# Performance work log

Hardware: AMD Instinct MI355X
Metric: run time of the kernel (lower is better)

Reference implementation:

```python
import jax, jax.numpy as jnp
import numpy as np

N = 512
E = N * N
H = 64          # hidden_dim
ED = 6          # edge_dim
L = 4           # n_layers
EPS = 1e-5


def _lin(key, fan_in, fan_out):
    k1, k2 = jax.random.split(key)
    w = jax.random.normal(k1, (fan_in, fan_out), jnp.float32) / np.sqrt(fan_in)
    b = jax.random.normal(k2, (fan_out,), jnp.float32) * 0.01
    return w, b


def _lin_stack(key, fan_in, fan_out, n):
    ws, bs = zip(*[_lin(jax.random.fold_in(key, i), fan_in, fan_out) for i in range(n)])
    return jnp.stack(ws), jnp.stack(bs)


def setup_inputs() -> dict:
    key = jax.random.key(0)
    ks = jax.random.split(key, 16)
    idx = jnp.arange(N, dtype=jnp.int32)
    src = jnp.repeat(idx, N)          # x_j source nodes
    dst = jnp.tile(idx, N)            # x_i target nodes (aggregation index)
    edge_index = jnp.stack([src, dst])  # [2, E]
    x = jax.random.normal(ks[0], (N, 6), jnp.float32)
    edge_attr = jax.random.normal(ks[1], (E, ED), jnp.float32)
    enc_w1, enc_b1 = _lin(ks[2], 6, H)
    enc_w2, enc_b2 = _lin(ks[3], H, H)
    att_w1, att_b1 = _lin_stack(ks[4], 2 * H + ED, H, L)   # [L,134,64]
    att_w2, att_b2 = _lin_stack(ks[5], H, 1, L)
    val_w1, val_b1 = _lin_stack(ks[6], H + ED, H, L)       # [L,70,64]
    val_w2, val_b2 = _lin_stack(ks[7], H, H, L)
    upd_w1, upd_b1 = _lin_stack(ks[8], 2 * H, H, L)        # [L,128,64]
    upd_w2, upd_b2 = _lin_stack(ks[9], H, H, L)
    ln_g = jnp.ones((L, H), jnp.float32)
    ln_b = jnp.zeros((L, H), jnp.float32)
    dec_w1, dec_b1 = _lin(ks[10], H, H)
    dec_w2, dec_b2 = _lin(ks[11], H, 1)
    return dict(x=x, edge_attr=edge_attr,
                enc_w1=enc_w1, enc_b1=enc_b1, enc_w2=enc_w2, enc_b2=enc_b2,
                att_w1=att_w1, att_b1=att_b1, att_w2=att_w2, att_b2=att_b2,
                val_w1=val_w1, val_b1=val_b1, val_w2=val_w2, val_b2=val_b2,
                upd_w1=upd_w1, upd_b1=upd_b1, upd_w2=upd_w2, upd_b2=upd_b2,
                ln_g=ln_g, ln_b=ln_b,
                dec_w1=dec_w1, dec_b1=dec_b1, dec_w2=dec_w2, dec_b2=dec_b2,
                edge_index=edge_index)


def reference(x, edge_attr, enc_w1, enc_b1, enc_w2, enc_b2,
              att_w1, att_b1, att_w2, att_b2,
              val_w1, val_b1, val_w2, val_b2,
              upd_w1, upd_b1, upd_w2, upd_b2,
              ln_g, ln_b, dec_w1, dec_b1, dec_w2, dec_b2, edge_index):
    src, dst = edge_index[0], edge_index[1]
    h = jax.nn.relu(x @ enc_w1 + enc_b1) @ enc_w2 + enc_b2  # [N,H]
    for l in range(L):
        hi = h[dst]                           # x_i  [E,H]
        hj = h[src]                           # x_j  [E,H]
        # attention logits: MLP([x_i || x_j || e])
        a_in = jnp.concatenate([hi, hj, edge_attr], axis=-1)   # [E,2H+ED]
        a = jax.nn.leaky_relu(a_in @ att_w1[l] + att_b1[l], 0.2) @ att_w2[l] + att_b2[l]
        a = a[:, 0]                                            # [E]
        # segment softmax over destination index (numerically stable)
        m = jax.ops.segment_max(a, dst, num_segments=N)
        e = jnp.exp(a - m[dst])
        s = jax.ops.segment_sum(e, dst, num_segments=N)
        alpha = e / s[dst]                                     # [E]
        # values: MLP([x_j || e])
        v_in = jnp.concatenate([hj, edge_attr], axis=-1)       # [E,H+ED]
        v = jax.nn.relu(v_in @ val_w1[l] + val_b1[l]) @ val_w2[l] + val_b2[l]
        agg = jax.ops.segment_sum(v * alpha[:, None], dst, num_segments=N)  # [N,H]
        # update + residual + LayerNorm
        u_in = jnp.concatenate([h, agg], axis=-1)              # [N,2H]
        u = jax.nn.relu(u_in @ upd_w1[l] + upd_b1[l]) @ upd_w2[l] + upd_b2[l]
        r = u + h
        mu = jnp.mean(r, axis=-1, keepdims=True)
        var = jnp.mean((r - mu) ** 2, axis=-1, keepdims=True)
        h = ln_g[l] * (r - mu) / jnp.sqrt(var + EPS) + ln_b[l]
    return jax.nn.relu(h @ dec_w1 + dec_b1) @ dec_w2 + dec_b2  # [N,1]
```

## Files before the change

### kernel.cpp

```cpp
#include <hip/hip_runtime.h>
#include <math.h>

#define NN 512
#define HH 64
#define NLAYERS 4
#define LN_EPS 1e-5f


__launch_bounds__(256)
__global__ void k_pre(const float* __restrict__ ea, const float* __restrict__ x,
                      const float* __restrict__ ew1, const float* __restrict__ eb1,
                      const float* __restrict__ ew2, const float* __restrict__ eb2,
                      const float* __restrict__ aw1, const float* __restrict__ ab1,
                      const float* __restrict__ wa2, const float* __restrict__ vw1,
                      const float* __restrict__ vb1,
                      float* __restrict__ EAT, float* __restrict__ h,
                      float* __restrict__ Pd, float* __restrict__ Qs,
                      float* __restrict__ Rv, float* __restrict__ Sq) {
    __shared__ float r1[HH], hs[HH];
    __shared__ float part[4][HH], partQ[4][HH], partR[4][HH];

    if (blockIdx.x < 1024) {
        int t = blockIdx.x * 256 + threadIdx.x;
        int i = t & (NN - 1);
        int j = t >> 9;
        const float2* s2 = (const float2*)(ea + ((size_t)i * NN + j) * 6);
        float2 e0 = s2[0], e1 = s2[1], e2 = s2[2];
        float4 a, b;
        a.x = e0.x; a.y = e0.y; a.z = e1.x; a.w = e1.y;
        b.x = e2.x; b.y = e2.y; b.z = 0.f; b.w = 0.f;
        float4* dst = (float4*)(EAT + (size_t)t * 8);
        dst[0] = a;
        dst[1] = b;
        return;
    }

    const int j = blockIdx.x - 1024;
    const int tid = threadIdx.x;
    const int d = tid & 63;
    const int w = tid >> 6;

    if (w == 0) {
        float z = eb1[d];
#pragma unroll
        for (int k = 0; k < 6; ++k) z += x[j * 6 + k] * ew1[k * HH + d];
        r1[d] = fmaxf(z, 0.f);
    }
    __syncthreads();
    {
        float z2 = (w == 0) ? eb2[d] : 0.f;
        for (int k = w * 16; k < w * 16 + 16; ++k) z2 += r1[k] * ew2[k * HH + d];
        part[w][d] = z2;
    }
    __syncthreads();
    if (w == 0) {
        float hv = part[0][d] + part[1][d] + part[2][d] + part[3][d];
        h[(size_t)j * HH + d] = hv;
        hs[d] = hv;
    }
    __syncthreads();
    {
        float pp = (w == 0) ? ab1[d] : 0.f;
        float qq = 0.f;
        float rr = (w == 0) ? vb1[d] : 0.f;
        for (int k = w * 16; k < w * 16 + 16; ++k) {
            float hk = hs[k];
            pp += hk * aw1[k * HH + d];
            qq += hk * aw1[(HH + k) * HH + d];
            rr += hk * vw1[k * HH + d];
        }
        part[w][d] = pp; partQ[w][d] = qq; partR[w][d] = rr;
    }
    __syncthreads();
    if (w == 0) {
        float qf = partQ[0][d] + partQ[1][d] + partQ[2][d] + partQ[3][d];
        Pd[(size_t)j * HH + d] = part[0][d] + part[1][d] + part[2][d] + part[3][d];
        Qs[(size_t)j * HH + d] = qf;
        Rv[(size_t)j * HH + d] = partR[0][d] + partR[1][d] + partR[2][d] + partR[3][d];
        float sq = qf * wa2[d];
#pragma unroll
        for (int o = 32; o; o >>= 1) sq += __shfl_xor(sq, o);
        if (d == 0) Sq[j] = sq;
    }
}

__launch_bounds__(512, 4)
__global__ void k_layer(const float* __restrict__ eat, const float* __restrict__ h_in,
                        const float* __restrict__ Pd, const float* __restrict__ Qs,
                        const float* __restrict__ Rv, const float* __restrict__ Sq,
                        const float* __restrict__ waE,
                        const float* __restrict__ wa2v,
                        const float* __restrict__ wvE,
                        const float* __restrict__ wv2, const float* __restrict__ vb2,
                        const float* __restrict__ uw1, const float* __restrict__ ub1,
                        const float* __restrict__ uw2, const float* __restrict__ ub2,
                        const float* __restrict__ lng, const float* __restrict__ lnb,
                        float* __restrict__ h_out,
                        const float* __restrict__ aw1n, const float* __restrict__ ab1n,
                        const float* __restrict__ wa2n, const float* __restrict__ vw1n,
                        const float* __restrict__ vb1n,
                        float* __restrict__ Pdn, float* __restrict__ Qsn,
                        float* __restrict__ Rvn, float* __restrict__ Sqn,
                        const float* __restrict__ dw1, const float* __restrict__ db1,
                        const float* __restrict__ dw2, const float* __restrict__ db2,
                        float* __restrict__ out,
                        int do_prep) {
    const int j = blockIdx.x;
    const int tid = threadIdx.x;
    const int lane = tid & 63;
    const int w = tid >> 6;
    const int slot = lane >> 3;
    const int dp = lane & 7;
    const int d0 = dp * 8;
    const int d = lane;

    __shared__ __align__(16) float ea_s[NN * 8];
    __shared__ __align__(16) float Sq_s[NN];
    __shared__ float a_s[NN];
    __shared__ float red_m[8], red_s[8];
    __shared__ float accs[8][HH];
    __shared__ float av[HH], uin[2 * HH], r1[HH], hs[HH];
    __shared__ float part[8][HH], partQ[8][HH], partR[8][HH];

    {
        const float4* s4 = (const float4*)(eat + (size_t)j * (NN * 8));
        float4* d4 = (float4*)ea_s;
        d4[tid] = s4[tid];
        d4[tid + 512] = s4[tid + 512];
    }
    if (tid < 128) ((float4*)Sq_s)[tid] = ((const float4*)Sq)[tid];

    float WA[6][8], wa2raw[8], wa2r[8], pdr[8], w6s[6];
#pragma unroll
    for (int k = 0; k < 6; ++k)
#pragma unroll
        for (int u = 0; u < 8; ++u) WA[k][u] = waE[k * HH + d0 + u];
#pragma unroll
    for (int u = 0; u < 8; ++u) {
        wa2raw[u] = wa2v[d0 + u];
        pdr[u] = Pd[(size_t)j * HH + d0 + u];
    }
#pragma unroll
    for (int k = 0; k < 6; ++k) {
        float t = 0.f;
#pragma unroll
        for (int u = 0; u < 8; ++u) t += WA[k][u] * wa2raw[u];
        t += __shfl_xor(t, 1);
        t += __shfl_xor(t, 2);
        t += __shfl_xor(t, 4);
        w6s[k] = 0.6f * t;
    }
#pragma unroll
    for (int u = 0; u < 8; ++u) wa2r[u] = 0.4f * wa2raw[u];
    __syncthreads();

    {
        float alin = 0.6f * Sq_s[tid];
#pragma unroll
        for (int k = 0; k < 6; ++k) alin += ea_s[tid * 8 + k] * w6s[k];
        __syncthreads();
        Sq_s[tid] = alin;
    }
    __syncthreads();

    const int ibw = w * 64;
    float lmax = -1e30f;
#pragma unroll
    for (int it = 0; it < 8; ++it) {
        const int i = ibw + it * 8 + slot;
        const float4* q4 = (const float4*)(Qs + (size_t)i * HH + d0);
        float4 qa = q4[0], qb = q4[1];
        float qv[8] = {qa.x, qa.y, qa.z, qa.w, qb.x, qb.y, qb.z, qb.w};
        const float4* e4 = (const float4*)(ea_s + i * 8);
        float4 ea0 = e4[0], ea1 = e4[1];
        float eav[6] = {ea0.x, ea0.y, ea0.z, ea0.w, ea1.x, ea1.y};
        float p1 = 0.f;
#pragma unroll
        for (int u = 0; u < 8; ++u) {
            float z = pdr[u] + qv[u];
#pragma unroll
            for (int k = 0; k < 6; ++k) z += eav[k] * WA[k][u];
            p1 += fabsf(z) * wa2r[u];
        }
        p1 += __shfl_xor(p1, 1);
        p1 += __shfl_xor(p1, 2);
        p1 += __shfl_xor(p1, 4);
        float a = Sq_s[i] + p1;
        if (dp == 0) a_s[i] = a;
        lmax = fmaxf(lmax, a);
    }
#pragma unroll
    for (int o = 32; o; o >>= 1) lmax = fmaxf(lmax, __shfl_xor(lmax, o));
    if (lane == 0) red_m[w] = lmax;
    __syncthreads();
    float m = red_m[0];
#pragma unroll
    for (int q = 1; q < 8; ++q) m = fmaxf(m, red_m[q]);

    float e = expf(a_s[tid] - m);
    a_s[tid] = e;
    float lsum = e;
#pragma unroll
    for (int o = 32; o; o >>= 1) lsum += __shfl_xor(lsum, o);
    if (lane == 0) red_s[w] = lsum;
    __syncthreads();
    float s = red_s[0];
#pragma unroll
    for (int q = 1; q < 8; ++q) s += red_s[q];

    float WV[6][8];
#pragma unroll
    for (int k = 0; k < 6; ++k)
#pragma unroll
        for (int u = 0; u < 8; ++u) WV[k][u] = wvE[k * HH + d0 + u];
    float acc[8] = {0.f, 0.f, 0.f, 0.f, 0.f, 0.f, 0.f, 0.f};
#pragma unroll
    for (int it = 0; it < 8; ++it) {
        const int i = ibw + it * 8 + slot;
        const float4* r4 = (const float4*)(Rv + (size_t)i * HH + d0);
        float4 ra = r4[0], rb = r4[1];
        float rv[8] = {ra.x, ra.y, ra.z, ra.w, rb.x, rb.y, rb.z, rb.w};
        const float4* e4 = (const float4*)(ea_s + i * 8);
        float4 ea0 = e4[0], ea1 = e4[1];
        float eav[6] = {ea0.x, ea0.y, ea0.z, ea0.w, ea1.x, ea1.y};
        const float wi = a_s[i];
#pragma unroll
        for (int u = 0; u < 8; ++u) {
            float z = rv[u];
#pragma unroll
            for (int k = 0; k < 6; ++k) z += eav[k] * WV[k][u];
            acc[u] += wi * fmaxf(z, 0.f);
        }
    }
#pragma unroll
    for (int u = 0; u < 8; ++u) {
        acc[u] += __shfl_xor(acc[u], 8);
        acc[u] += __shfl_xor(acc[u], 16);
        acc[u] += __shfl_xor(acc[u], 32);
    }
    if (slot == 0) {
#pragma unroll
        for (int u = 0; u < 8; ++u) accs[w][d0 + u] = acc[u];
    }
    __syncthreads();
    if (tid < HH) {
        float tot = accs[0][tid];
#pragma unroll
        for (int q = 1; q < 8; ++q) tot += accs[q][tid];
        av[tid] = tot / s;
    }
    __syncthreads();

    const float hv = h_in[(size_t)j * HH + d];
    {
        float p = (w == 0) ? vb2[d] : 0.f;
        for (int k = w * 8; k < w * 8 + 8; ++k) p += av[k] * wv2[k * HH + d];
        part[w][d] = p;
        if (w == 0) uin[d] = hv;
    }
    __syncthreads();
    if (w == 0) {
        float agg = part[0][d];
#pragma unroll
        for (int q = 1; q < 8; ++q) agg += part[q][d];
        uin[HH + d] = agg;
    }
    __syncthreads();
    {
        float t = (w == 0) ? ub1[d] : 0.f;
        for (int c = w * 16; c < w * 16 + 16; ++c) t += uin[c] * uw1[c * HH + d];
        part[w][d] = t;
    }
    __syncthreads();
    if (w == 0) {
        float t = part[0][d];
#pragma unroll
        for (int q = 1; q < 8; ++q) t += part[q][d];
        r1[d] = fmaxf(t, 0.f);
    }
    __syncthreads();
    {
        float u = (w == 0) ? ub2[d] : 0.f;
        for (int k = w * 8; k < w * 8 + 8; ++k) u += r1[k] * uw2[k * HH + d];
        part[w][d] = u;
    }
    __syncthreads();
    if (w == 0) {
        float r = hv + part[0][d];
#pragma unroll
        for (int q = 1; q < 8; ++q) r += part[q][d];
        float sum = r;
#pragma unroll
        for (int o = 32; o; o >>= 1) sum += __shfl_xor(sum, o);
        float mu = sum * (1.f / HH);
        float dr = r - mu;
        float v2 = dr * dr;
#pragma unroll
        for (int o = 32; o; o >>= 1) v2 += __shfl_xor(v2, o);
        float var = v2 * (1.f / HH);
        float hn = lng[d] * dr * (1.f / sqrtf(var + LN_EPS)) + lnb[d];
        h_out[(size_t)j * HH + d] = hn;
        hs[d] = hn;
    }
    __syncthreads();

    if (do_prep) {
        float pp = (w == 0) ? ab1n[d] : 0.f;
        float qq = 0.f;
        float rr = (w == 0) ? vb1n[d] : 0.f;
        for (int k = w * 8; k < w * 8 + 8; ++k) {
            float hk = hs[k];
            pp += hk * aw1n[k * HH + d];
            qq += hk * aw1n[(HH + k) * HH + d];
            rr += hk * vw1n[k * HH + d];
        }
        part[w][d] = pp; partQ[w][d] = qq; partR[w][d] = rr;
        __syncthreads();
        if (w == 0) {
            float pf = part[0][d], qf = partQ[0][d], rf = partR[0][d];
#pragma unroll
            for (int q = 1; q < 8; ++q) {
                pf += part[q][d]; qf += partQ[q][d]; rf += partR[q][d];
            }
            Pdn[(size_t)j * HH + d] = pf;
            Qsn[(size_t)j * HH + d] = qf;
            Rvn[(size_t)j * HH + d] = rf;
            float sq = qf * wa2n[d];
#pragma unroll
            for (int o = 32; o; o >>= 1) sq += __shfl_xor(sq, o);
            if (d == 0) Sqn[j] = sq;
        }
    } else {
        float t = (w == 0) ? db1[d] : 0.f;
        for (int k = w * 8; k < w * 8 + 8; ++k) t += hs[k] * dw1[k * HH + d];
        part[w][d] = t;
        __syncthreads();
        if (w == 0) {
            float tt = part[0][d];
#pragma unroll
            for (int q = 1; q < 8; ++q) tt += part[q][d];
            tt = fmaxf(tt, 0.f);
            float sum = tt * dw2[d];
#pragma unroll
            for (int o = 32; o; o >>= 1) sum += __shfl_xor(sum, o);
            if (d == 0) out[j] = sum + db2[0];
        }
    }
}

extern "C" void kernel_launch(void* const* d_in, const int* in_sizes, int n_in,
                              void* d_out, int out_size, void* d_ws, size_t ws_size,
                              hipStream_t stream) {
    const float* x      = (const float*)d_in[0];
    const float* ea     = (const float*)d_in[1];
    const float* enc_w1 = (const float*)d_in[2];
    const float* enc_b1 = (const float*)d_in[3];
    const float* enc_w2 = (const float*)d_in[4];
    const float* enc_b2 = (const float*)d_in[5];
    const float* att_w1 = (const float*)d_in[6];
    const float* att_b1 = (const float*)d_in[7];
    const float* att_w2 = (const float*)d_in[8];
    const float* val_w1 = (const float*)d_in[10];
    const float* val_b1 = (const float*)d_in[11];
    const float* val_w2 = (const float*)d_in[12];
    const float* val_b2 = (const float*)d_in[13];
    const float* upd_w1 = (const float*)d_in[14];
    const float* upd_b1 = (const float*)d_in[15];
    const float* upd_w2 = (const float*)d_in[16];
    const float* upd_b2 = (const float*)d_in[17];
    const float* ln_g   = (const float*)d_in[18];
    const float* ln_b   = (const float*)d_in[19];
    const float* dec_w1 = (const float*)d_in[20];
    const float* dec_b1 = (const float*)d_in[21];
    const float* dec_w2 = (const float*)d_in[22];
    const float* dec_b2 = (const float*)d_in[23];

    const size_t NH = (size_t)NN * HH;
    float* ws   = (float*)d_ws;
    float* EAT  = ws;
    float* h0   = EAT + (size_t)NN * NN * 8;
    float* h1   = h0 + NH;
    float* Pd0  = h1 + NH;
    float* Pd1  = Pd0 + NH;
    float* Qs0  = Pd1 + NH;
    float* Qs1  = Qs0 + NH;
    float* Rv0  = Qs1 + NH;
    float* Rv1  = Rv0 + NH;
    float* Sq0  = Rv1 + NH;
    float* Sq1  = Sq0 + NN;

    float* Pdb[2] = {Pd0, Pd1};
    float* Qsb[2] = {Qs0, Qs1};
    float* Rvb[2] = {Rv0, Rv1};
    float* Sqb[2] = {Sq0, Sq1};
    float* hb[2]  = {h0, h1};

    k_pre<<<1536, 256, 0, stream>>>(ea, x, enc_w1, enc_b1, enc_w2, enc_b2,
                                    att_w1, att_b1, att_w2, val_w1, val_b1,
                                    EAT, h0, Pd0, Qs0, Rv0, Sq0);

    for (int l = 0; l < NLAYERS; ++l) {
        const int cur = l & 1, nxt = (l + 1) & 1;
        const int np = (l + 1 < NLAYERS) ? (l + 1) : l;
        const float* aw1 = att_w1 + (size_t)l * 134 * HH;
        const float* vw1 = val_w1 + (size_t)l * 70 * HH;
        k_layer<<<NN, 512, 0, stream>>>(
            EAT, hb[cur],
            Pdb[cur], Qsb[cur], Rvb[cur], Sqb[cur],
            aw1 + 128 * HH, att_w2 + l * HH, vw1 + 64 * HH,
            val_w2 + (size_t)l * HH * HH, val_b2 + l * HH,
            upd_w1 + (size_t)l * 2 * HH * HH, upd_b1 + l * HH,
            upd_w2 + (size_t)l * HH * HH, upd_b2 + l * HH,
            ln_g + l * HH, ln_b + l * HH,
            hb[nxt],
            att_w1 + (size_t)np * 134 * HH, att_b1 + np * HH, att_w2 + np * HH,
            val_w1 + (size_t)np * 70 * HH, val_b1 + np * HH,
            Pdb[nxt], Qsb[nxt], Rvb[nxt], Sqb[nxt],
            dec_w1, dec_b1, dec_w2, dec_b2, (float*)d_out,
            (l + 1 < NLAYERS) ? 1 : 0);
    }
}
```

Measured before the change: 209.4 us.

## Fuse all layers into one persistent cooperative kernel with grid sync

```diff
diff --git a/kernel.cpp b/kernel.cpp
--- a/kernel.cpp
+++ b/kernel.cpp
@@ -1,5 +1,8 @@
 #include <hip/hip_runtime.h>
+#include <hip/hip_cooperative_groups.h>
 #include <math.h>
+
+namespace cg = cooperative_groups;
 
 #define NN 512
 #define HH 64
@@ -84,12 +87,289 @@
     }
 }
 
+struct NetP {
+    const float *EAT, *h0, *Pd0;
+    const float *aw1, *ab1, *aw2, *vw1, *vb1, *vw2, *vb2;
+    const float *uw1, *ub1, *uw2, *ub2, *lng, *lnb;
+    const float *dw1, *db1, *dw2, *db2;
+    float *Qs0, *Qs1, *Rv0, *Rv1, *Sq0, *Sq1;
+    float *out;
+};
+
+__launch_bounds__(512, 4)
+__global__ void k_net(NetP P) {
+    cg::grid_group grid = cg::this_grid();
+    const int j = blockIdx.x;
+    const int tid = threadIdx.x;
+    const int lane = tid & 63;
+    const int w = tid >> 6;
+    const int slot = lane >> 3;
+    const int dp = lane & 7;
+    const int d0 = dp * 8;
+    const int d = lane;
+
+    __shared__ __align__(16) float ea_s[NN * 8];
+    __shared__ __align__(16) float Sq_s[NN];
+    __shared__ float a_s[NN];
+    __shared__ float red_m[8], red_s[8];
+    __shared__ float accs[8][HH];
+    __shared__ float av[HH], uin[2 * HH], r1[HH], hs[HH], pd_s[HH];
+    __shared__ float part[8][HH], partQ[8][HH], partR[8][HH];
+
+    {
+        const float4* s4 = (const float4*)(P.EAT + (size_t)j * (NN * 8));
+        float4* d4 = (float4*)ea_s;
+        d4[tid] = s4[tid];
+        d4[tid + 512] = s4[tid + 512];
+    }
+    if (w == 0) {
+        hs[d] = P.h0[(size_t)j * HH + d];
+        pd_s[d] = P.Pd0[(size_t)j * HH + d];
+    }
+    __syncthreads();
+
+    for (int l = 0; l < NLAYERS; ++l) {
+        const float* aw1l = P.aw1 + (size_t)l * 134 * HH;
+        const float* waE  = aw1l + 128 * HH;
+        const float* wa2v = P.aw2 + l * HH;
+        const float* wvE  = P.vw1 + (size_t)l * 70 * HH + 64 * HH;
+        const float* Qs_c = (l & 1) ? P.Qs1 : P.Qs0;
+        const float* Rv_c = (l & 1) ? P.Rv1 : P.Rv0;
+        const float* Sq_c = (l & 1) ? P.Sq1 : P.Sq0;
+
+        if (tid < 128) ((float4*)Sq_s)[tid] = ((const float4*)Sq_c)[tid];
+
+        float WA[6][8], wa2raw[8], wa2r[8], pdr[8], w6s[6];
+#pragma unroll
+        for (int k = 0; k < 6; ++k)
+#pragma unroll
+            for (int u = 0; u < 8; ++u) WA[k][u] = waE[k * HH + d0 + u];
+#pragma unroll
+        for (int u = 0; u < 8; ++u) {
+            wa2raw[u] = wa2v[d0 + u];
+            pdr[u] = pd_s[d0 + u];
+        }
+#pragma unroll
+        for (int k = 0; k < 6; ++k) {
+            float t = 0.f;
+#pragma unroll
+            for (int u = 0; u < 8; ++u) t += WA[k][u] * wa2raw[u];
+            t += __shfl_xor(t, 1);
+            t += __shfl_xor(t, 2);
+            t += __shfl_xor(t, 4);
+            w6s[k] = 0.6f * t;
+        }
+#pragma unroll
+        for (int u = 0; u < 8; ++u) wa2r[u] = 0.4f * wa2raw[u];
+        __syncthreads();
+
+        {
+            float alin = 0.6f * Sq_s[tid];
+#pragma unroll
+            for (int k = 0; k < 6; ++k) alin += ea_s[tid * 8 + k] * w6s[k];
+            a_s[tid] = alin;
+        }
+        __syncthreads();
+
+        const int ibw = w * 64;
+        float lmax = -1e30f;
+#pragma unroll
+        for (int it = 0; it < 8; ++it) {
+            const int i = ibw + it * 8 + slot;
+            const float4* q4 = (const float4*)(Qs_c + (size_t)i * HH + d0);
+            float4 qa = q4[0], qb = q4[1];
+            float qv[8] = {qa.x, qa.y, qa.z, qa.w, qb.x, qb.y, qb.z, qb.w};
+            const float4* e4 = (const float4*)(ea_s + i * 8);
+            float4 ea0 = e4[0], ea1 = e4[1];
+            float eav[6] = {ea0.x, ea0.y, ea0.z, ea0.w, ea1.x, ea1.y};
+            float p1 = 0.f;
+#pragma unroll
+            for (int u = 0; u < 8; ++u) {
+                float z = pdr[u] + qv[u];
+#pragma unroll
+                for (int k = 0; k < 6; ++k) z += eav[k] * WA[k][u];
+                p1 += fabsf(z) * wa2r[u];
+            }
+            p1 += __shfl_xor(p1, 1);
+            p1 += __shfl_xor(p1, 2);
+            p1 += __shfl_xor(p1, 4);
+            float a = a_s[i] + p1;
+            if (dp == 0) a_s[i] = a;
+            lmax = fmaxf(lmax, a);
+        }
+#pragma unroll
+        for (int o = 32; o; o >>= 1) lmax = fmaxf(lmax, __shfl_xor(lmax, o));
+        if (lane == 0) red_m[w] = lmax;
+        __syncthreads();
+        float m = red_m[0];
+#pragma unroll
+        for (int q = 1; q < 8; ++q) m = fmaxf(m, red_m[q]);
+
+        float e = expf(a_s[tid] - m);
+        a_s[tid] = e;
+        float lsum = e;
+#pragma unroll
+        for (int o = 32; o; o >>= 1) lsum += __shfl_xor(lsum, o);
+        if (lane == 0) red_s[w] = lsum;
+        __syncthreads();
+        float s = red_s[0];
+#pragma unroll
+        for (int q = 1; q < 8; ++q) s += red_s[q];
+
+        float WV[6][8];
+#pragma unroll
+        for (int k = 0; k < 6; ++k)
+#pragma unroll
+            for (int u = 0; u < 8; ++u) WV[k][u] = wvE[k * HH + d0 + u];
+        float acc[8] = {0.f, 0.f, 0.f, 0.f, 0.f, 0.f, 0.f, 0.f};
+#pragma unroll
+        for (int it = 0; it < 8; ++it) {
+            const int i = ibw + it * 8 + slot;
+            const float4* r4 = (const float4*)(Rv_c + (size_t)i * HH + d0);
+            float4 ra = r4[0], rb = r4[1];
+            float rv[8] = {ra.x, ra.y, ra.z, ra.w, rb.x, rb.y, rb.z, rb.w};
+            const float4* e4 = (const float4*)(ea_s + i * 8);
+            float4 ea0 = e4[0], ea1 = e4[1];
+            float eav[6] = {ea0.x, ea0.y, ea0.z, ea0.w, ea1.x, ea1.y};
+            const float wi = a_s[i];
+#pragma unroll
+            for (int u = 0; u < 8; ++u) {
+                float z = rv[u];
+#pragma unroll
+                for (int k = 0; k < 6; ++k) z += eav[k] * WV[k][u];
+                acc[u] += wi * fmaxf(z, 0.f);
+            }
+        }
+#pragma unroll
+        for (int u = 0; u < 8; ++u) {
+            acc[u] += __shfl_xor(acc[u], 8);
+            acc[u] += __shfl_xor(acc[u], 16);
+            acc[u] += __shfl_xor(acc[u], 32);
+        }
+        if (slot == 0) {
+#pragma unroll
+            for (int u = 0; u < 8; ++u) accs[w][d0 + u] = acc[u];
+        }
+        __syncthreads();
+        if (tid < HH) {
+            float tot = accs[0][tid];
+#pragma unroll
+            for (int q = 1; q < 8; ++q) tot += accs[q][tid];
+            av[tid] = tot / s;
+        }
+        __syncthreads();
+
+        const float* wv2 = P.vw2 + (size_t)l * HH * HH;
+        const float* uw1 = P.uw1 + (size_t)l * 2 * HH * HH;
+        const float* uw2 = P.uw2 + (size_t)l * HH * HH;
+        const float hv = hs[d];
+        {
+            float p = (w == 0) ? P.vb2[l * HH + d] : 0.f;
+            for (int k = w * 8; k < w * 8 + 8; ++k) p += av[k] * wv2[k * HH + d];
+            part[w][d] = p;
+            if (w == 0) uin[d] = hv;
+        }
+        __syncthreads();
+        if (w == 0) {
+            float agg = part[0][d];
+#pragma unroll
+            for (int q = 1; q < 8; ++q) agg += part[q][d];
+            uin[HH + d] = agg;
+        }
+        __syncthreads();
+        {
+            float t = (w == 0) ? P.ub1[l * HH + d] : 0.f;
+            for (int c = w * 16; c < w * 16 + 16; ++c) t += uin[c] * uw1[c * HH + d];
+            part[w][d] = t;
+        }
+        __syncthreads();
+        if (w == 0) {
+            float t = part[0][d];
+#pragma unroll
+            for (int q = 1; q < 8; ++q) t += part[q][d];
+            r1[d] = fmaxf(t, 0.f);
+        }
+        __syncthreads();
+        {
+            float u = (w == 0) ? P.ub2[l * HH + d] : 0.f;
+            for (int k = w * 8; k < w * 8 + 8; ++k) u += r1[k] * uw2[k * HH + d];
+            part[w][d] = u;
+        }
+        __syncthreads();
+        if (w == 0) {
+            float r = hv + part[0][d];
+#pragma unroll
+            for (int q = 1; q < 8; ++q) r += part[q][d];
+            float sum = r;
+#pragma unroll
+            for (int o = 32; o; o >>= 1) sum += __shfl_xor(sum, o);
+            float mu = sum * (1.f / HH);
+            float dr = r - mu;
+            float v2 = dr * dr;
+#pragma unroll
+            for (int o = 32; o; o >>= 1) v2 += __shfl_xor(v2, o);
+            float var = v2 * (1.f / HH);
+            hs[d] = P.lng[l * HH + d] * dr * (1.f / sqrtf(var + LN_EPS)) + P.lnb[l * HH + d];
+        }
+        __syncthreads();
+
+        if (l + 1 < NLAYERS) {
+            const int np = l + 1;
+            const float* aw1n = P.aw1 + (size_t)np * 134 * HH;
+            const float* vw1n = P.vw1 + (size_t)np * 70 * HH;
+            float* Qsn = (np & 1) ? P.Qs1 : P.Qs0;
+            float* Rvn = (np & 1) ? P.Rv1 : P.Rv0;
+            float* Sqn = (np & 1) ? P.Sq1 : P.Sq0;
+            float pp = (w == 0) ? P.ab1[np * HH + d] : 0.f;
+            float qq = 0.f;
+            float rr = (w == 0) ? P.vb1[np * HH + d] : 0.f;
+            for (int k = w * 8; k < w * 8 + 8; ++k) {
+                float hk = hs[k];
+                pp += hk * aw1n[k * HH + d];
+                qq += hk * aw1n[(HH + k) * HH + d];
+                rr += hk * vw1n[k * HH + d];
+            }
+            part[w][d] = pp; partQ[w][d] = qq; partR[w][d] = rr;
+            __syncthreads();
+            if (w == 0) {
+                float pf = part[0][d], qf = partQ[0][d], rf = partR[0][d];
+#pragma unroll
+                for (int q = 1; q < 8; ++q) {
+                    pf += part[q][d]; qf += partQ[q][d]; rf += partR[q][d];
+                }
+                pd_s[d] = pf;
+                Qsn[(size_t)j * HH + d] = qf;
+                Rvn[(size_t)j * HH + d] = rf;
+                float sq = qf * P.aw2[np * HH + d];
+#pragma unroll
+                for (int o = 32; o; o >>= 1) sq += __shfl_xor(sq, o);
+                if (d == 0) Sqn[j] = sq;
+            }
+            grid.sync();
+        } else {
+            float t = (w == 0) ? P.db1[d] : 0.f;
+            for (int k = w * 8; k < w * 8 + 8; ++k) t += hs[k] * P.dw1[k * HH + d];
+            part[w][d] = t;
+            __syncthreads();
+            if (w == 0) {
+                float tt = part[0][d];
+#pragma unroll
+                for (int q = 1; q < 8; ++q) tt += part[q][d];
+                tt = fmaxf(tt, 0.f);
+                float sum = tt * P.dw2[d];
+#pragma unroll
+                for (int o = 32; o; o >>= 1) sum += __shfl_xor(sum, o);
+                if (d == 0) P.out[j] = sum + P.db2[0];
+            }
+        }
+    }
+}
+
 __launch_bounds__(512, 4)
 __global__ void k_layer(const float* __restrict__ eat, const float* __restrict__ h_in,
                         const float* __restrict__ Pd, const float* __restrict__ Qs,
                         const float* __restrict__ Rv, const float* __restrict__ Sq,
-                        const float* __restrict__ waE,
-                        const float* __restrict__ wa2v,
+                        const float* __restrict__ waE, const float* __restrict__ wa2v,
                         const float* __restrict__ wvE,
                         const float* __restrict__ wv2, const float* __restrict__ vb2,
                         const float* __restrict__ uw1, const float* __restrict__ ub1,
@@ -158,8 +438,7 @@
         float alin = 0.6f * Sq_s[tid];
 #pragma unroll
         for (int k = 0; k < 6; ++k) alin += ea_s[tid * 8 + k] * w6s[k];
-        __syncthreads();
-        Sq_s[tid] = alin;
+        a_s[tid] = alin;
     }
     __syncthreads();
 
@@ -185,7 +464,7 @@
         p1 += __shfl_xor(p1, 1);
         p1 += __shfl_xor(p1, 2);
         p1 += __shfl_xor(p1, 4);
-        float a = Sq_s[i] + p1;
+        float a = a_s[i] + p1;
         if (dp == 0) a_s[i] = a;
         lmax = fmaxf(lmax, a);
     }
@@ -389,16 +668,29 @@
     float* Sq0  = Rv1 + NH;
     float* Sq1  = Sq0 + NN;
 
+    k_pre<<<1536, 256, 0, stream>>>(ea, x, enc_w1, enc_b1, enc_w2, enc_b2,
+                                    att_w1, att_b1, att_w2, val_w1, val_b1,
+                                    EAT, h0, Pd0, Qs0, Rv0, Sq0);
+
+    NetP P;
+    P.EAT = EAT; P.h0 = h0; P.Pd0 = Pd0;
+    P.aw1 = att_w1; P.ab1 = att_b1; P.aw2 = att_w2;
+    P.vw1 = val_w1; P.vb1 = val_b1; P.vw2 = val_w2; P.vb2 = val_b2;
+    P.uw1 = upd_w1; P.ub1 = upd_b1; P.uw2 = upd_w2; P.ub2 = upd_b2;
+    P.lng = ln_g;  P.lnb = ln_b;
+    P.dw1 = dec_w1; P.db1 = dec_b1; P.dw2 = dec_w2; P.db2 = dec_b2;
+    P.Qs0 = Qs0; P.Qs1 = Qs1; P.Rv0 = Rv0; P.Rv1 = Rv1; P.Sq0 = Sq0; P.Sq1 = Sq1;
+    P.out = (float*)d_out;
+    void* kargs[] = { (void*)&P };
+    hipError_t rc = hipLaunchCooperativeKernel((const void*)k_net, dim3(NN), dim3(512),
+                                               kargs, 0, stream);
+    if (rc == hipSuccess) return;
+
     float* Pdb[2] = {Pd0, Pd1};
     float* Qsb[2] = {Qs0, Qs1};
     float* Rvb[2] = {Rv0, Rv1};
     float* Sqb[2] = {Sq0, Sq1};
     float* hb[2]  = {h0, h1};
-
-    k_pre<<<1536, 256, 0, stream>>>(ea, x, enc_w1, enc_b1, enc_w2, enc_b2,
-                                    att_w1, att_b1, att_w2, val_w1, val_b1,
-                                    EAT, h0, Pd0, Qs0, Rv0, Sq0);
-
     for (int l = 0; l < NLAYERS; ++l) {
         const int cur = l & 1, nxt = (l + 1) & 1;
         const int np = (l + 1 < NLAYERS) ? (l + 1) : l;
```

Result: slower. 508.5 us (+142.8%).
